# Optimization experiments

Measured on AMD Instinct MI355X. Metric: run time of the kernel, lower is better.

Reference implementation:

```python
import jax, jax.numpy as jnp
import numpy as np

B, N, C = 4, 2048, 768
H = 12
DH = C // H
HID = int(C * 4.0)
SCALE = DH ** -0.5
EPS = 1e-5


def layernorm(x, g, b):
    mu = jnp.mean(x, axis=-1, keepdims=True)
    var = jnp.var(x, axis=-1, keepdims=True)
    return (x - mu) * jax.lax.rsqrt(var + EPS) * g + b


def setup_inputs() -> dict:
    key = jax.random.key(0)
    ks = jax.random.split(key, 10)
    s = lambda fan_in: 1.0 / np.sqrt(fan_in)
    return {
        "x": jax.random.normal(ks[0], (B, N, C), dtype=jnp.float32),
        "ln1_g": jnp.ones((C,), jnp.float32),
        "ln1_b": jnp.zeros((C,), jnp.float32),
        "w_qkv": jax.random.uniform(ks[1], (C, 3 * C), jnp.float32, -s(C), s(C)),
        "w_proj": jax.random.uniform(ks[2], (C, C), jnp.float32, -s(C), s(C)),
        "b_proj": jnp.zeros((C,), jnp.float32),
        "ln2_g": jnp.ones((C,), jnp.float32),
        "ln2_b": jnp.zeros((C,), jnp.float32),
        "w_fc1": jax.random.uniform(ks[3], (C, HID), jnp.float32, -s(C), s(C)),
        "b_fc1": jnp.zeros((HID,), jnp.float32),
        "w_fc2": jax.random.uniform(ks[4], (HID, C), jnp.float32, -s(HID), s(HID)),
        "b_fc2": jnp.zeros((C,), jnp.float32),
    }


def reference(x, ln1_g, ln1_b, w_qkv, w_proj, b_proj, ln2_g, ln2_b, w_fc1, b_fc1, w_fc2, b_fc2):
    # --- attention branch ---
    h = layernorm(x, ln1_g, ln1_b)                       # [B,N,C]
    qkv = (h @ w_qkv).reshape(B, N, 3, H, DH)
    q = qkv[:, :, 0].transpose(0, 2, 1, 3)               # [B,H,N,DH]
    k = qkv[:, :, 1].transpose(0, 2, 1, 3)
    v = qkv[:, :, 2].transpose(0, 2, 1, 3)
    attn = jnp.einsum('bhnd,bhmd->bhnm', q, k) * SCALE   # [B,H,N,N]
    attn = jax.nn.softmax(attn, axis=-1)
    y = jnp.einsum('bhnm,bhmd->bhnd', attn, v)           # [B,H,N,DH]
    y = y.transpose(0, 2, 1, 3).reshape(B, N, C)
    y = y @ w_proj + b_proj
    x = x + y
    # --- MLP branch ---
    h = layernorm(x, ln2_g, ln2_b)
    h = jax.nn.gelu(h @ w_fc1 + b_fc1, approximate=False)
    h = h @ w_fc2 + b_fc2
    return x + h
```

## Files before the change

kernel.cpp:

```cpp
#include <hip/hip_runtime.h>
#include <stdint.h>

#define DEV __device__ __forceinline__

typedef __attribute__((ext_vector_type(8))) short bf16x8;
typedef __attribute__((ext_vector_type(4))) float f32x4;
typedef __attribute__((ext_vector_type(4))) short s16x4;

DEV short f2bf(float f) {
    union { float f; unsigned u; } v; v.f = f;
    unsigned r = v.u + 0x7fffu + ((v.u >> 16) & 1u);
    return (short)(r >> 16);
}

DEV uint32_t cvtpk(float lo, float hi) {
    uint32_t r;
    asm("v_cvt_pk_bf16_f32 %0, %1, %2" : "=v"(r) : "v"(lo), "v"(hi));
    return r;
}

typedef const unsigned int __attribute__((address_space(1)))* gp1;
typedef unsigned int __attribute__((address_space(3)))* lp3;

DEV void gload16(const void* g, void* l) {
    __builtin_amdgcn_global_load_lds((gp1)g, (lp3)l, 16, 0, 0);
}

DEV void wait4_barrier() { asm volatile("s_waitcnt vmcnt(4)\ns_barrier" ::: "memory"); }
DEV void wait2_barrier() { asm volatile("s_waitcnt vmcnt(2)\ns_barrier" ::: "memory"); }
DEV void wait0_barrier() { asm volatile("s_waitcnt vmcnt(0)\ns_barrier" ::: "memory"); }

__global__ __launch_bounds__(256) void tcvt(
    const float* __restrict__ W, short* __restrict__ WT, int K, int N)
{
    __shared__ float t[32][33];
    int n0 = blockIdx.x * 32, k0 = blockIdx.y * 32;
    int tx = threadIdx.x & 31, ty = threadIdx.x >> 5;
#pragma unroll
    for (int i = 0; i < 32; i += 8)
        t[ty + i][tx] = W[(size_t)(k0 + ty + i) * N + n0 + tx];
    __syncthreads();
#pragma unroll
    for (int i = 0; i < 32; i += 8)
        WT[(size_t)(n0 + ty + i) * K + k0 + tx] = f2bf(t[tx][ty + i]);
}

__global__ __launch_bounds__(256) void ln_bf16(
    const float* __restrict__ x, const float* __restrict__ gam,
    const float* __restrict__ bet, short* __restrict__ out)
{
    const int w = threadIdx.x >> 6, lane = threadIdx.x & 63;
    const size_t row = (size_t)blockIdx.x * 4 + w;
    const float* xr = x + row * 768;
    float4 v[3];
    float s = 0.f, ss = 0.f;
#pragma unroll
    for (int k = 0; k < 3; ++k) {
        v[k] = *(const float4*)(xr + k * 256 + lane * 4);
        s  += v[k].x + v[k].y + v[k].z + v[k].w;
        ss += v[k].x * v[k].x + v[k].y * v[k].y + v[k].z * v[k].z + v[k].w * v[k].w;
    }
#pragma unroll
    for (int i = 1; i < 64; i <<= 1) { s += __shfl_xor(s, i, 64); ss += __shfl_xor(ss, i, 64); }
    const float inv = 1.f / 768.f;
    float mu = s * inv;
    float var = ss * inv - mu * mu;
    float rstd = rsqrtf(var + 1e-5f);
#pragma unroll
    for (int k = 0; k < 3; ++k) {
        int c = k * 256 + lane * 4;
        float vv[4] = { v[k].x, v[k].y, v[k].z, v[k].w };
        s16x4 o;
#pragma unroll
        for (int j = 0; j < 4; ++j)
            o[j] = f2bf((vv[j] - mu) * rstd * gam[c + j] + bet[c + j]);
        *(s16x4*)(out + row * 768 + c) = o;
    }
}

template<int MODE>
__global__ __launch_bounds__(256, 3) void gemm_bf16(
    const short* __restrict__ A, const short* __restrict__ Bt,
    int M, int N, int K,
    const float* __restrict__ bias, const float* __restrict__ resid,
    float* __restrict__ outf, short* __restrict__ outb,
    short* __restrict__ qo, short* __restrict__ ko, short* __restrict__ vo)
{
    __shared__ __align__(16) short As[3][128 * 32];
    __shared__ __align__(16) short Bs[3][128 * 32];
    const int tid = threadIdx.x;
    const int w = tid >> 6, lane = tid & 63;
    const int g = lane >> 4, l15 = lane & 15;
    const int brow = blockIdx.x * 128, bcol = blockIdx.y * 128;
    const int wr = w >> 1, wc = w & 1;
    f32x4 acc[4][4] = {};

    auto stage = [&](int buf, int kt) {
#pragma unroll
        for (int c = 0; c < 2; ++c) {
            int base = w * 2048 + c * 1024;
            int L = base + lane * 16;
            int r = L >> 6;
            int b = L & 63;
            int bs = b ^ (((r >> 1) & 3) << 4);
            gload16((const char*)(A  + (size_t)(brow + r) * K + kt) + bs, (char*)&As[buf][0] + base);
            gload16((const char*)(Bt + (size_t)(bcol + r) * K + kt) + bs, (char*)&Bs[buf][0] + base);
        }
    };

    const int KT = K >> 5;
    stage(0, 0);
    stage(1, 32);
    wait4_barrier();

    int cur = 0;
    for (int ki = 0; ki < KT; ++ki) {
        if (ki + 2 < KT) {
            int nxt2 = cur + 2; if (nxt2 >= 3) nxt2 -= 3;
            stage(nxt2, (ki + 2) << 5);
        }
        bf16x8 af[4], bfg[4];
#pragma unroll
        for (int m = 0; m < 4; ++m) {
            int r = wr * 64 + m * 16 + l15;
            af[m] = *(const bf16x8*)((const char*)&As[cur][0] + r * 64 + ((g * 16) ^ (((r >> 1) & 3) << 4)));
        }
#pragma unroll
        for (int n = 0; n < 4; ++n) {
            int r = wc * 64 + n * 16 + l15;
            bfg[n] = *(const bf16x8*)((const char*)&Bs[cur][0] + r * 64 + ((g * 16) ^ (((r >> 1) & 3) << 4)));
        }
#pragma unroll
        for (int m = 0; m < 4; ++m)
#pragma unroll
            for (int n = 0; n < 4; ++n)
                acc[m][n] = __builtin_amdgcn_mfma_f32_16x16x32_bf16(af[m], bfg[n], acc[m][n], 0, 0, 0);
        if (ki + 1 < KT) {
            if (ki + 2 < KT) wait4_barrier();
            else             wait0_barrier();
        }
        ++cur; if (cur >= 3) cur -= 3;
    }

#pragma unroll
    for (int m = 0; m < 4; ++m) {
#pragma unroll
        for (int n = 0; n < 4; ++n) {
#pragma unroll
            for (int j = 0; j < 4; ++j) {
                int r = brow + wr * 64 + m * 16 + g * 4 + j;
                int c = bcol + wc * 64 + n * 16 + l15;
                float v = acc[m][n][j];
                if (MODE == 0) {
                    int which = c / 768, cc = c % 768;
                    int h = cc >> 6, d = cc & 63;
                    int b_ = r >> 11, nn = r & 2047;
                    size_t bh = (size_t)b_ * 12 + h;
                    if (which == 0)      qo[(bh * 2048 + nn) * 64 + d] = f2bf(v * 0.18033688011112042f);
                    else if (which == 1) ko[(bh * 2048 + nn) * 64 + d] = f2bf(v);
                    else                 vo[(bh * 64 + d) * 2048 + nn] = f2bf(v);
                } else if (MODE == 1) {
                    outf[(size_t)r * N + c] = v + bias[c] + resid[(size_t)r * N + c];
                } else {
                    float t = v + bias[c];
                    float ge = 0.5f * t * (1.0f + erff(t * 0.70710678118654752f));
                    outb[(size_t)r * N + c] = f2bf(ge);
                }
            }
        }
    }
}

__global__ __launch_bounds__(256, 4) void attn_fwd(
    const short* __restrict__ Q, const short* __restrict__ Kg,
    const short* __restrict__ Vt, short* __restrict__ Y)
{
    __shared__ __align__(16) short Kl[4][32 * 64];
    __shared__ __align__(16) short Vl[4][64 * 32];
    __shared__ __align__(16) short Pl[4][32 * 32];
    const int tid = threadIdx.x, w = tid >> 6, lane = tid & 63;
    const int g = lane >> 4, l15 = lane & 15;
    const int bh = blockIdx.y;
    const int q0 = blockIdx.x * 128 + w * 32;
    const short* Qb = Q  + (size_t)bh * 2048 * 64;
    const short* Kb = Kg + (size_t)bh * 2048 * 64;
    const short* Vb = Vt + (size_t)bh * 64 * 2048;

    bf16x8 qf[2][2];
#pragma unroll
    for (int m = 0; m < 2; ++m)
#pragma unroll
        for (int kk = 0; kk < 2; ++kk)
            qf[m][kk] = *(const bf16x8*)(Qb + (size_t)(q0 + m * 16 + l15) * 64 + kk * 32 + g * 8);

    f32x4 accO[2][4] = {};
    float lpart[2] = { 0.f, 0.f };

    auto stage = [&](int buf, int k0) {
        int bb = w * 1024;
        int L = bb + lane * 16;
        int rk = L >> 7, bk_ = L & 127;
        int bsk = bk_ ^ ((rk & 7) << 4);
        gload16((const char*)(Kb + (size_t)(k0 + rk) * 64) + bsk, (char*)(&Kl[buf][0]) + bb);
        int rv = L >> 6, bv = L & 63;
        int bsv = bv ^ (((rv >> 1) & 3) << 4);
        gload16((const char*)(Vb + (size_t)rv * 2048 + k0) + bsv, (char*)(&Vl[buf][0]) + bb);
    };

    stage(0, 0);
    stage(1, 32);
    stage(2, 64);
    wait4_barrier();

    for (int t = 0; t < 64; ++t) {
        const int cur = t & 3;
        if (t + 3 < 64) stage((t + 3) & 3, (t + 3) * 32);
        const char* Kc = (const char*)&Kl[cur][0];
        const char* Vc = (const char*)&Vl[cur][0];

        f32x4 s[2][2] = {};
        __builtin_amdgcn_s_setprio(1);
#pragma unroll
        for (int kk = 0; kk < 2; ++kk) {
            bf16x8 kf[2];
#pragma unroll
            for (int n = 0; n < 2; ++n) {
                int key = n * 16 + l15;
                kf[n] = *(const bf16x8*)(Kc + key * 128 +
                         ((kk * 64 + g * 16) ^ ((key & 7) << 4)));
            }
#pragma unroll
            for (int m = 0; m < 2; ++m)
#pragma unroll
                for (int n = 0; n < 2; ++n)
                    s[m][n] = __builtin_amdgcn_mfma_f32_16x16x32_bf16(kf[n], qf[m][kk], s[m][n], 0, 0, 0);
        }
        __builtin_amdgcn_s_setprio(0);

        short* P = &Pl[w][0];
#pragma unroll
        for (int m = 0; m < 2; ++m) {
            int qr = m * 16 + l15;
            char* prow = (char*)P + qr * 64;
            int sw = ((qr >> 1) & 3) << 4;
#pragma unroll
            for (int n = 0; n < 2; ++n) {
                float e0 = __builtin_amdgcn_exp2f(s[m][n][0]);
                float e1 = __builtin_amdgcn_exp2f(s[m][n][1]);
                float e2 = __builtin_amdgcn_exp2f(s[m][n][2]);
                float e3 = __builtin_amdgcn_exp2f(s[m][n][3]);
                lpart[m] += (e0 + e1) + (e2 + e3);
                int keyb = n * 32 + g * 8;
                uint2 pk; pk.x = cvtpk(e0, e1); pk.y = cvtpk(e2, e3);
                *(uint2*)(prow + (keyb ^ sw)) = pk;
            }
        }

        __builtin_amdgcn_s_setprio(1);
        {
            bf16x8 vf[4], pf[2];
#pragma unroll
            for (int n = 0; n < 4; ++n) {
                int d = n * 16 + l15;
                vf[n] = *(const bf16x8*)(Vc + d * 64 + ((g * 16) ^ (((d >> 1) & 3) << 4)));
            }
#pragma unroll
            for (int m = 0; m < 2; ++m) {
                int qr = m * 16 + l15;
                pf[m] = *(const bf16x8*)((const char*)P + qr * 64 + ((g * 16) ^ (((qr >> 1) & 3) << 4)));
            }
#pragma unroll
            for (int m = 0; m < 2; ++m)
#pragma unroll
                for (int n = 0; n < 4; ++n)
                    accO[m][n] = __builtin_amdgcn_mfma_f32_16x16x32_bf16(pf[m], vf[n], accO[m][n], 0, 0, 0);
        }
        __builtin_amdgcn_s_setprio(0);

        if (t < 61)      wait4_barrier();
        else if (t == 61) wait2_barrier();
        else if (t == 62) wait0_barrier();
    }

#pragma unroll
    for (int m = 0; m < 2; ++m) {
        lpart[m] += __shfl_xor(lpart[m], 16, 64);
        lpart[m] += __shfl_xor(lpart[m], 32, 64);
    }

    int b_ = bh / 12, h = bh % 12;
#pragma unroll
    for (int m = 0; m < 2; ++m) {
        float linv[4];
#pragma unroll
        for (int j = 0; j < 4; ++j)
            linv[j] = 1.0f / __shfl(lpart[m], g * 4 + j, 64);
#pragma unroll
        for (int n = 0; n < 4; ++n)
#pragma unroll
            for (int j = 0; j < 4; ++j) {
                int qq = q0 + m * 16 + g * 4 + j;
                int d = n * 16 + l15;
                Y[((size_t)b_ * 2048 + qq) * 768 + h * 64 + d] = f2bf(accO[m][n][j] * linv[j]);
            }
    }
}

extern "C" void kernel_launch(void* const* d_in, const int* in_sizes, int n_in,
                              void* d_out, int out_size, void* d_ws, size_t ws_size,
                              hipStream_t stream)
{
    const float* x      = (const float*)d_in[0];
    const float* ln1_g  = (const float*)d_in[1];
    const float* ln1_b  = (const float*)d_in[2];
    const float* w_qkv  = (const float*)d_in[3];
    const float* w_proj = (const float*)d_in[4];
    const float* b_proj = (const float*)d_in[5];
    const float* ln2_g  = (const float*)d_in[6];
    const float* ln2_b  = (const float*)d_in[7];
    const float* w_fc1  = (const float*)d_in[8];
    const float* b_fc1  = (const float*)d_in[9];
    const float* w_fc2  = (const float*)d_in[10];
    const float* b_fc2  = (const float*)d_in[11];

    char* ws = (char*)d_ws;
    size_t off = 0;
    auto alloc = [&](size_t bytes) -> void* {
        void* p = ws + off; off += (bytes + 255) & ~(size_t)255; return p;
    };
    short* wqkvT = (short*)alloc((size_t)2304 * 768 * 2);
    short* wprojT= (short*)alloc((size_t)768 * 768 * 2);
    short* wfc1T = (short*)alloc((size_t)3072 * 768 * 2);
    short* wfc2T = (short*)alloc((size_t)768 * 3072 * 2);
    short* h1    = (short*)alloc((size_t)8192 * 768 * 2);
    short* qb    = (short*)alloc((size_t)48 * 2048 * 64 * 2);
    short* kb    = (short*)alloc((size_t)48 * 2048 * 64 * 2);
    short* vtb   = (short*)alloc((size_t)48 * 64 * 2048 * 2);
    short* yb    = (short*)alloc((size_t)8192 * 768 * 2);
    float* X1    = (float*)alloc((size_t)8192 * 768 * 4);
    short* h2    = (short*)alloc((size_t)8192 * 768 * 2);
    short* h3    = (short*)alloc((size_t)8192 * 3072 * 2);

    tcvt<<<dim3(2304 / 32, 768 / 32),  256, 0, stream>>>(w_qkv,  wqkvT,  768,  2304);
    tcvt<<<dim3(768 / 32,  768 / 32),  256, 0, stream>>>(w_proj, wprojT, 768,  768);
    tcvt<<<dim3(3072 / 32, 768 / 32),  256, 0, stream>>>(w_fc1,  wfc1T,  768,  3072);
    tcvt<<<dim3(768 / 32,  3072 / 32), 256, 0, stream>>>(w_fc2,  wfc2T,  3072, 768);

    ln_bf16<<<2048, 256, 0, stream>>>(x, ln1_g, ln1_b, h1);

    gemm_bf16<0><<<dim3(64, 18), 256, 0, stream>>>(h1, wqkvT, 8192, 2304, 768,
        nullptr, nullptr, nullptr, nullptr, qb, kb, vtb);

    attn_fwd<<<dim3(16, 48), 256, 0, stream>>>(qb, kb, vtb, yb);

    gemm_bf16<1><<<dim3(64, 6), 256, 0, stream>>>(yb, wprojT, 8192, 768, 768,
        b_proj, x, X1, nullptr, nullptr, nullptr, nullptr);

    ln_bf16<<<2048, 256, 0, stream>>>(X1, ln2_g, ln2_b, h2);

    gemm_bf16<2><<<dim3(64, 24), 256, 0, stream>>>(h2, wfc1T, 8192, 3072, 768,
        b_fc1, nullptr, nullptr, h3, nullptr, nullptr, nullptr);

    gemm_bf16<1><<<dim3(64, 6), 256, 0, stream>>>(h3, wfc2T, 8192, 768, 3072,
        b_fc2, X1, (float*)d_out, nullptr, nullptr, nullptr, nullptr);
}
```

Baseline: 309.2 us.

## Use 256x256 8-wave GEMM with staged double-buffered K=64 tiles for QKV and FC1

Adds a new gemm256 kernel with 256x256 output tiles, 512 threads, 128KB dynamic LDS and K-step 64. Loads are split into four phases interleaved with MFMA work and barriers, and setprio is raised around the MFMAs. The kernel is used for the QKV and FC1 projections, while the residual-add GEMMs keep the old 128x128 kernel. The aim is more operand reuse per LDS load and better overlap of loads with compute, at the cost of fewer blocks (288/384 on 256 CUs), which gives wave-quantization and occupancy risk.

```diff
diff --git a/kernel.cpp b/kernel.cpp
--- a/kernel.cpp
+++ b/kernel.cpp
@@ -26,6 +26,7 @@
     __builtin_amdgcn_global_load_lds((gp1)g, (lp3)l, 16, 0, 0);
 }
 
+DEV void bar()           { asm volatile("s_barrier" ::: "memory"); }
 DEV void wait4_barrier() { asm volatile("s_waitcnt vmcnt(4)\ns_barrier" ::: "memory"); }
 DEV void wait2_barrier() { asm volatile("s_waitcnt vmcnt(2)\ns_barrier" ::: "memory"); }
 DEV void wait0_barrier() { asm volatile("s_waitcnt vmcnt(0)\ns_barrier" ::: "memory"); }
@@ -79,76 +80,108 @@
 }
 
 template<int MODE>
-__global__ __launch_bounds__(256, 3) void gemm_bf16(
+__global__ __launch_bounds__(512, 2) void gemm256(
     const short* __restrict__ A, const short* __restrict__ Bt,
     int M, int N, int K,
-    const float* __restrict__ bias, const float* __restrict__ resid,
-    float* __restrict__ outf, short* __restrict__ outb,
+    const float* __restrict__ bias,
+    short* __restrict__ outb,
     short* __restrict__ qo, short* __restrict__ ko, short* __restrict__ vo)
 {
-    __shared__ __align__(16) short As[3][128 * 32];
-    __shared__ __align__(16) short Bs[3][128 * 32];
+    extern __shared__ __align__(16) char smem[];
+    char* const AsB[2] = { smem,         smem + 32768 };
+    char* const BsB[2] = { smem + 65536, smem + 98304 };
     const int tid = threadIdx.x;
     const int w = tid >> 6, lane = tid & 63;
     const int g = lane >> 4, l15 = lane & 15;
-    const int brow = blockIdx.x * 128, bcol = blockIdx.y * 128;
-    const int wr = w >> 1, wc = w & 1;
-    f32x4 acc[4][4] = {};
-
-    auto stage = [&](int buf, int kt) {
-#pragma unroll
-        for (int c = 0; c < 2; ++c) {
-            int base = w * 2048 + c * 1024;
-            int L = base + lane * 16;
-            int r = L >> 6;
-            int b = L & 63;
-            int bs = b ^ (((r >> 1) & 3) << 4);
-            gload16((const char*)(A  + (size_t)(brow + r) * K + kt) + bs, (char*)&As[buf][0] + base);
-            gload16((const char*)(Bt + (size_t)(bcol + r) * K + kt) + bs, (char*)&Bs[buf][0] + base);
-        }
-    };
-
-    const int KT = K >> 5;
-    stage(0, 0);
-    stage(1, 32);
-    wait4_barrier();
-
-    int cur = 0;
-    for (int ki = 0; ki < KT; ++ki) {
-        if (ki + 2 < KT) {
-            int nxt2 = cur + 2; if (nxt2 >= 3) nxt2 -= 3;
-            stage(nxt2, (ki + 2) << 5);
-        }
-        bf16x8 af[4], bfg[4];
-#pragma unroll
-        for (int m = 0; m < 4; ++m) {
-            int r = wr * 64 + m * 16 + l15;
-            af[m] = *(const bf16x8*)((const char*)&As[cur][0] + r * 64 + ((g * 16) ^ (((r >> 1) & 3) << 4)));
-        }
+    const int wr = w >> 2, wc = w & 3;
+    const int brow = blockIdx.x * 256, bcol = blockIdx.y * 256;
+    const int wbase = w * 1024;
+
+    f32x4 acc[8][4] = {};
+
+    auto stageA = [&](int buf, int kt, int c) {
+        int base = c * 8192 + wbase;
+        int L = base + lane * 16;
+        int r = L >> 7, b = L & 127;
+        int bs = b ^ ((r & 7) << 4);
+        gload16((const char*)(A + (size_t)(brow + r) * K + kt * 64) + bs, AsB[buf] + base);
+    };
+    auto stageB = [&](int buf, int kt, int c) {
+        int base = c * 8192 + wbase;
+        int L = base + lane * 16;
+        int r = L >> 7, b = L & 127;
+        int bs = b ^ ((r & 7) << 4);
+        gload16((const char*)(Bt + (size_t)(bcol + r) * K + kt * 64) + bs, BsB[buf] + base);
+    };
+    auto ldA = [&](int buf, int m, int kk) -> bf16x8 {
+        int r = wr * 128 + m * 16 + l15;
+        int off = (kk * 64 + g * 16) ^ ((r & 7) << 4);
+        return *(const bf16x8*)(AsB[buf] + r * 128 + off);
+    };
+    auto ldB = [&](int buf, int n, int kk) -> bf16x8 {
+        int r = wc * 64 + n * 16 + l15;
+        int off = (kk * 64 + g * 16) ^ ((r & 7) << 4);
+        return *(const bf16x8*)(BsB[buf] + r * 128 + off);
+    };
+
+    const int NT = K >> 6;
+
+    stageA(0, 0, 0); stageA(0, 0, 1); stageA(0, 0, 2); stageA(0, 0, 3);
+    stageB(0, 0, 0); stageB(0, 0, 1); stageB(0, 0, 2); stageB(0, 0, 3);
+    stageA(1, 1, 0); stageA(1, 1, 2);
+    wait2_barrier();
+
+    bf16x8 bfr[4][2];
+
+#define PHASE(BUF, Q, STAGES) do {                                             \
+    bf16x8 a0 = ldA(BUF, 2*(Q),   0);                                          \
+    bf16x8 a1 = ldA(BUF, 2*(Q),   1);                                          \
+    bf16x8 a2 = ldA(BUF, 2*(Q)+1, 0);                                          \
+    bf16x8 a3 = ldA(BUF, 2*(Q)+1, 1);                                          \
+    if ((Q) == 0) {                                                            \
+        _Pragma("unroll")                                                      \
+        for (int n = 0; n < 4; ++n) {                                          \
+            bfr[n][0] = ldB(BUF, n, 0);                                        \
+            bfr[n][1] = ldB(BUF, n, 1);                                        \
+        }                                                                      \
+    }                                                                          \
+    STAGES;                                                                    \
+    bar();                                                                     \
+    __builtin_amdgcn_s_setprio(1);                                             \
+    _Pragma("unroll")                                                          \
+    for (int n = 0; n < 4; ++n) {                                              \
+        acc[2*(Q)][n]   = __builtin_amdgcn_mfma_f32_16x16x32_bf16(a0, bfr[n][0], acc[2*(Q)][n],   0, 0, 0); \
+        acc[2*(Q)][n]   = __builtin_amdgcn_mfma_f32_16x16x32_bf16(a1, bfr[n][1], acc[2*(Q)][n],   0, 0, 0); \
+        acc[2*(Q)+1][n] = __builtin_amdgcn_mfma_f32_16x16x32_bf16(a2, bfr[n][0], acc[2*(Q)+1][n], 0, 0, 0); \
+        acc[2*(Q)+1][n] = __builtin_amdgcn_mfma_f32_16x16x32_bf16(a3, bfr[n][1], acc[2*(Q)+1][n], 0, 0, 0); \
+    }                                                                          \
+    __builtin_amdgcn_s_setprio(0);                                             \
+} while (0)
+
+#define TILE(BUF, U) do {                                                      \
+    PHASE(BUF, 0, if ((U)+1 < NT) { stageA((BUF)^1, (U)+1, 1); stageA((BUF)^1, (U)+1, 3); }); \
+    bar();                                                                     \
+    PHASE(BUF, 1, if ((U)+1 < NT) { stageB((BUF)^1, (U)+1, 0); stageB((BUF)^1, (U)+1, 1); }); \
+    bar();                                                                     \
+    PHASE(BUF, 2, if ((U)+1 < NT) { stageB((BUF)^1, (U)+1, 2); stageB((BUF)^1, (U)+1, 3); }); \
+    bar();                                                                     \
+    PHASE(BUF, 3, if ((U)+2 < NT) { stageA((BUF),   (U)+2, 0); stageA((BUF),   (U)+2, 2); }); \
+    if ((U)+2 < NT)      wait2_barrier();                                      \
+    else if ((U)+1 < NT) wait0_barrier();                                      \
+    else                 bar();                                                \
+} while (0)
+
+    for (int tt = 0; tt < NT; tt += 2) { TILE(0, tt); TILE(1, tt + 1); }
+#undef PHASE
+#undef TILE
+
+#pragma unroll
+    for (int m = 0; m < 8; ++m) {
 #pragma unroll
         for (int n = 0; n < 4; ++n) {
-            int r = wc * 64 + n * 16 + l15;
-            bfg[n] = *(const bf16x8*)((const char*)&Bs[cur][0] + r * 64 + ((g * 16) ^ (((r >> 1) & 3) << 4)));
-        }
-#pragma unroll
-        for (int m = 0; m < 4; ++m)
-#pragma unroll
-            for (int n = 0; n < 4; ++n)
-                acc[m][n] = __builtin_amdgcn_mfma_f32_16x16x32_bf16(af[m], bfg[n], acc[m][n], 0, 0, 0);
-        if (ki + 1 < KT) {
-            if (ki + 2 < KT) wait4_barrier();
-            else             wait0_barrier();
-        }
-        ++cur; if (cur >= 3) cur -= 3;
-    }
-
-#pragma unroll
-    for (int m = 0; m < 4; ++m) {
-#pragma unroll
-        for (int n = 0; n < 4; ++n) {
 #pragma unroll
             for (int j = 0; j < 4; ++j) {
-                int r = brow + wr * 64 + m * 16 + g * 4 + j;
+                int r = brow + wr * 128 + m * 16 + g * 4 + j;
                 int c = bcol + wc * 64 + n * 16 + l15;
                 float v = acc[m][n][j];
                 if (MODE == 0) {
@@ -159,8 +192,6 @@
                     if (which == 0)      qo[(bh * 2048 + nn) * 64 + d] = f2bf(v * 0.18033688011112042f);
                     else if (which == 1) ko[(bh * 2048 + nn) * 64 + d] = f2bf(v);
                     else                 vo[(bh * 64 + d) * 2048 + nn] = f2bf(v);
-                } else if (MODE == 1) {
-                    outf[(size_t)r * N + c] = v + bias[c] + resid[(size_t)r * N + c];
                 } else {
                     float t = v + bias[c];
                     float ge = 0.5f * t * (1.0f + erff(t * 0.70710678118654752f));
@@ -169,6 +200,81 @@
             }
         }
     }
+}
+
+template<int MODE>
+__global__ __launch_bounds__(256, 3) void gemm_bf16(
+    const short* __restrict__ A, const short* __restrict__ Bt,
+    int M, int N, int K,
+    const float* __restrict__ bias, const float* __restrict__ resid,
+    float* __restrict__ outf)
+{
+    __shared__ __align__(16) short As[3][128 * 32];
+    __shared__ __align__(16) short Bs[3][128 * 32];
+    const int tid = threadIdx.x;
+    const int w = tid >> 6, lane = tid & 63;
+    const int g = lane >> 4, l15 = lane & 15;
+    const int brow = blockIdx.x * 128, bcol = blockIdx.y * 128;
+    const int wr = w >> 1, wc = w & 1;
+    f32x4 acc[4][4] = {};
+
+    auto stage = [&](int buf, int kt) {
+#pragma unroll
+        for (int c = 0; c < 2; ++c) {
+            int base = w * 2048 + c * 1024;
+            int L = base + lane * 16;
+            int r = L >> 6;
+            int b = L & 63;
+            int bs = b ^ (((r >> 1) & 3) << 4);
+            gload16((const char*)(A  + (size_t)(brow + r) * K + kt) + bs, (char*)&As[buf][0] + base);
+            gload16((const char*)(Bt + (size_t)(bcol + r) * K + kt) + bs, (char*)&Bs[buf][0] + base);
+        }
+    };
+
+    const int KT = K >> 5;
+    stage(0, 0);
+    stage(1, 32);
+    wait4_barrier();
+
+    int cur = 0;
+    for (int ki = 0; ki < KT; ++ki) {
+        if (ki + 2 < KT) {
+            int nxt2 = cur + 2; if (nxt2 >= 3) nxt2 -= 3;
+            stage(nxt2, (ki + 2) << 5);
+        }
+        bf16x8 af[4], bfg[4];
+#pragma unroll
+        for (int m = 0; m < 4; ++m) {
+            int r = wr * 64 + m * 16 + l15;
+            af[m] = *(const bf16x8*)((const char*)&As[cur][0] + r * 64 + ((g * 16) ^ (((r >> 1) & 3) << 4)));
+        }
+#pragma unroll
+        for (int n = 0; n < 4; ++n) {
+            int r = wc * 64 + n * 16 + l15;
+            bfg[n] = *(const bf16x8*)((const char*)&Bs[cur][0] + r * 64 + ((g * 16) ^ (((r >> 1) & 3) << 4)));
+        }
+#pragma unroll
+        for (int m = 0; m < 4; ++m)
+#pragma unroll
+            for (int n = 0; n < 4; ++n)
+                acc[m][n] = __builtin_amdgcn_mfma_f32_16x16x32_bf16(af[m], bfg[n], acc[m][n], 0, 0, 0);
+        if (ki + 1 < KT) {
+            if (ki + 2 < KT) wait4_barrier();
+            else             wait0_barrier();
+        }
+        ++cur; if (cur >= 3) cur -= 3;
+    }
+
+#pragma unroll
+    for (int m = 0; m < 4; ++m)
+#pragma unroll
+        for (int n = 0; n < 4; ++n)
+#pragma unroll
+            for (int j = 0; j < 4; ++j) {
+                int r = brow + wr * 64 + m * 16 + g * 4 + j;
+                int c = bcol + wc * 64 + n * 16 + l15;
+                outf[(size_t)r * N + c] = acc[m][n][j] + bias[c] + resid[(size_t)r * N + c];
+            }
 }
 
 __global__ __launch_bounds__(256, 4) void attn_fwd(
@@ -277,7 +383,7 @@
         }
         __builtin_amdgcn_s_setprio(0);
 
-        if (t < 61)      wait4_barrier();
+        if (t < 61)       wait4_barrier();
         else if (t == 61) wait2_barrier();
         else if (t == 62) wait0_barrier();
     }
@@ -341,6 +447,9 @@
     short* h2    = (short*)alloc((size_t)8192 * 768 * 2);
     short* h3    = (short*)alloc((size_t)8192 * 3072 * 2);
 
+    hipFuncSetAttribute((const void*)gemm256<0>, hipFuncAttributeMaxDynamicSharedMemorySize, 131072);
+    hipFuncSetAttribute((const void*)gemm256<2>, hipFuncAttributeMaxDynamicSharedMemorySize, 131072);
+
     tcvt<<<dim3(2304 / 32, 768 / 32),  256, 0, stream>>>(w_qkv,  wqkvT,  768,  2304);
     tcvt<<<dim3(768 / 32,  768 / 32),  256, 0, stream>>>(w_proj, wprojT, 768,  768);
     tcvt<<<dim3(3072 / 32, 768 / 32),  256, 0, stream>>>(w_fc1,  wfc1T,  768,  3072);
@@ -348,19 +457,19 @@
 
     ln_bf16<<<2048, 256, 0, stream>>>(x, ln1_g, ln1_b, h1);
 
-    gemm_bf16<0><<<dim3(64, 18), 256, 0, stream>>>(h1, wqkvT, 8192, 2304, 768,
-        nullptr, nullptr, nullptr, nullptr, qb, kb, vtb);
+    gemm256<0><<<dim3(32, 9), 512, 131072, stream>>>(h1, wqkvT, 8192, 2304, 768,
+        nullptr, nullptr, qb, kb, vtb);
 
     attn_fwd<<<dim3(16, 48), 256, 0, stream>>>(qb, kb, vtb, yb);
 
     gemm_bf16<1><<<dim3(64, 6), 256, 0, stream>>>(yb, wprojT, 8192, 768, 768,
-        b_proj, x, X1, nullptr, nullptr, nullptr, nullptr);
+        b_proj, x, X1);
 
     ln_bf16<<<2048, 256, 0, stream>>>(X1, ln2_g, ln2_b, h2);
 
-    gemm_bf16<2><<<dim3(64, 24), 256, 0, stream>>>(h2, wfc1T, 8192, 3072, 768,
-        b_fc1, nullptr, nullptr, h3, nullptr, nullptr, nullptr);
+    gemm256<2><<<dim3(32, 12), 512, 131072, stream>>>(h2, wfc1T, 8192, 3072, 768,
+        b_fc1, h3, nullptr, nullptr, nullptr);
 
     gemm_bf16<1><<<dim3(64, 6), 256, 0, stream>>>(h3, wfc2T, 8192, 768, 3072,
-        b_fc2, X1, (float*)d_out, nullptr, nullptr, nullptr, nullptr);
-}
+        b_fc2, X1, (float*)d_out);
+}
```

After: 400.9 us. 1.3x slower.
